# Kernel optimization log

Measured on AMD Instinct MI355X. Metric: run time of the kernel, lower is better.

Reference implementation:

```python
import jax, jax.numpy as jnp
import numpy as np

N, E, G = 50000, 600000, 500          # nodes, edges, graphs in batch
IN_NODE, HID, EDGE = 92, 64, 41       # CGCNN default feature dims
NCONV, PRED, NOUT = 3, 128, 1
Z_DIM = 2 * HID + EDGE                # 169: cat(src_x, dst_x, edge_attr)
BN_EPS = 1e-5


def setup_inputs() -> dict:
    key = jax.random.key(0)
    ks = jax.random.split(key, 14)
    f32 = jnp.float32
    return {
        "x": jax.random.normal(ks[0], (N, IN_NODE), f32),
        "edge_attr": jax.random.normal(ks[1], (E, EDGE), f32),
        "src": jax.random.randint(ks[2], (E,), 0, N),
        "dst": jax.random.randint(ks[3], (E,), 0, N),
        "graph_idx": jnp.sort(jax.random.randint(ks[4], (N,), 0, G)),
        "n_graphs": G,
        "W_embed": jax.random.normal(ks[5], (IN_NODE, HID), f32) / np.sqrt(IN_NODE),
        "b_embed": jnp.zeros((HID,), f32),
        "W_sig": jax.random.normal(ks[6], (NCONV, Z_DIM, HID), f32) / np.sqrt(Z_DIM),
        "b_sig": jnp.zeros((NCONV, HID), f32),
        "W_sp": jax.random.normal(ks[7], (NCONV, Z_DIM, HID), f32) / np.sqrt(Z_DIM),
        "b_sp": jnp.zeros((NCONV, HID), f32),
        "bn_gamma": jnp.ones((NCONV, HID), f32),
        "bn_beta": jnp.zeros((NCONV, HID), f32),
        "W_fc": jax.random.normal(ks[8], (HID, PRED), f32) / np.sqrt(HID),
        "b_fc": jnp.zeros((PRED,), f32),
        "W_out": jax.random.normal(ks[9], (PRED, NOUT), f32) / np.sqrt(PRED),
        "b_out": jnp.zeros((NOUT,), f32),
    }


def reference(x, edge_attr, src, dst, graph_idx, n_graphs,
              W_embed, b_embed, W_sig, b_sig, W_sp, b_sp,
              bn_gamma, bn_beta, W_fc, b_fc, W_out, b_out):
    # node embedding to hidden dim
    h = x @ W_embed + b_embed                                   # [N, HID]
    n_nodes = h.shape[0]
    for i in range(W_sig.shape[0]):
        # per-edge features: gather src/dst node feats + edge feats
        z = jnp.concatenate([h[src], h[dst], edge_attr], axis=1)  # [E, Z_DIM]
        gated = jax.nn.sigmoid(z @ W_sig[i] + b_sig[i])           # [E, HID]
        msg = jax.nn.softplus(z @ W_sp[i] + b_sp[i])              # [E, HID]
        # scatter-sum gated messages into destination node mailboxes
        agg = jax.ops.segment_sum(gated * msg, dst, num_segments=n_nodes)
        h = h + agg                                               # residual
        # batch norm over nodes (training-mode batch stats, biased var)
        mean = h.mean(axis=0)
        var = h.var(axis=0)
        h = (h - mean) * jax.lax.rsqrt(var + BN_EPS) * bn_gamma[i] + bn_beta[i]
    # sum-pool nodes per graph, then dense readout
    graph_feat = jax.ops.segment_sum(h, graph_idx, num_segments=n_graphs)  # [G, HID]
    graph_feat = graph_feat @ W_fc + b_fc                                  # [G, PRED]
    return graph_feat @ W_out + b_out                                      # [G, NOUT]
```

## Files before the change

### kernel.cpp

```cpp
#include <hip/hip_runtime.h>

#define N_NODES 50000
#define N_EDGES 600000
#define N_GRAPHS 500
#define IN_F 92
#define HID 64
#define EDGE_F 41
#define ZDIM 169
#define PRED 128
#define BN_EPS 1e-5f
#define SCAN_BLOCKS 196
#define ROW_U32 24
#define LOG2E 1.4426950408889634f
#define LN2   0.6931471805599453f
#define NAGG_BLOCKS 2048
#define NW2 (NAGG_BLOCKS * 8)
#define PART_T ((N_EDGES + 1 + NW2 - 1) / NW2)

typedef unsigned int u32;
typedef _Float16 f16;
typedef _Float16 f16x2 __attribute__((ext_vector_type(2)));
typedef _Float16 f16x8 __attribute__((ext_vector_type(8)));
typedef float f32x4 __attribute__((ext_vector_type(4)));

__device__ __forceinline__ u32 f2bf(float f) {
    u32 u = __float_as_uint(f);
    return (u + 0x7fffu + ((u >> 16) & 1u)) >> 16;
}

__device__ __forceinline__ int lbound(const int* __restrict__ a, int nelem, int val) {
    int lo = 0, hi = nelem;
    while (lo < hi) {
        int m = (lo + hi) >> 1;
        if (a[m] < val) lo = m + 1; else hi = m;
    }
    return lo;
}

__global__ void k_prep(const float* __restrict__ Wsig, const float* __restrict__ Wsp,
                       const float* __restrict__ Wemb, const int* __restrict__ gidx,
                       f16* __restrict__ Wf16, f16* __restrict__ Wp2,
                       f16* __restrict__ Wef, int* __restrict__ gstart,
                       int* __restrict__ zeroBase) {
    int t = blockIdx.x * 256 + threadIdx.x;
    if (t < 3072) {
        int lane = t & 63;
        int jt = (t >> 6) & 7;
        int kt = (t >> 9) & 1;
        int L = t >> 10;
        int j128 = jt * 16 + (lane & 15);
        const float* Wbase = (j128 < 64) ? Wsig : Wsp;
        int j = j128 & 63;
        f16x8 v;
        #pragma unroll
        for (int b = 0; b < 8; ++b) {
            int k = kt * 32 + (lane >> 4) * 8 + b;
            float f = (k < EDGE_F) ? Wbase[(size_t)L * ZDIM * HID + (128 + k) * HID + j] * LOG2E : 0.f;
            v[b] = (f16)f;
        }
        *(f16x8*)(Wf16 + ((size_t)((L * 2 + kt) * 8 + jt) * 64 + lane) * 8) = v;
    } else if (t < 9216) {
        int t2 = t - 3072;
        int lane = t2 & 63;
        int jt = (t2 >> 6) & 15;
        int kt = (t2 >> 10) & 1;
        int L = t2 >> 11;
        int j256 = jt * 16 + (lane & 15);
        const float* Wbase = (j256 & 64) ? Wsp : Wsig;
        int rowoff = (j256 & 128) ? 64 : 0;
        int j = j256 & 63;
        f16x8 v;
        #pragma unroll
        for (int b = 0; b < 8; ++b) {
            int k = kt * 32 + (lane >> 4) * 8 + b;
            v[b] = (f16)Wbase[(size_t)L * ZDIM * HID + (rowoff + k) * HID + j];
        }
        *(f16x8*)(Wp2 + ((size_t)((L * 2 + kt) * 16 + jt) * 64 + lane) * 8) = v;
    } else if (t < 9984) {
        int t3 = t - 9216;
        int lane = t3 & 63;
        int jt = (t3 >> 6) & 3;
        int kt = t3 >> 8;
        int j = jt * 16 + (lane & 15);
        f16x8 v;
        #pragma unroll
        for (int b = 0; b < 8; ++b) {
            int k = kt * 32 + (lane >> 4) * 8 + b;
            v[b] = (k < IN_F) ? (f16)Wemb[(size_t)k * HID + j] : (f16)0.f;
        }
        *(f16x8*)(Wef + ((size_t)(kt * 4 + jt) * 64 + lane) * 8) = v;
    } else if (t < 10485) {
        int g = t - 9984;
        gstart[g] = lbound(gidx, N_NODES, g);
    } else if (t < 10485 + 2 * N_NODES) {
        zeroBase[t - 10485] = 0;
    }
}

__global__ void k_hist(const int* __restrict__ dst, int* __restrict__ deg) {
    int e = blockIdx.x * 256 + threadIdx.x;
    if (e < N_EDGES) atomicAdd(&deg[dst[e]], 1);
}

__global__ __launch_bounds__(256) void k_scanA(const int* __restrict__ deg,
                                               int* __restrict__ partial) {
    __shared__ int s[256];
    int i = blockIdx.x * 256 + threadIdx.x;
    s[threadIdx.x] = (i < N_NODES) ? deg[i] : 0;
    __syncthreads();
    for (int off = 128; off > 0; off >>= 1) {
        if (threadIdx.x < off) s[threadIdx.x] += s[threadIdx.x + off];
        __syncthreads();
    }
    if (threadIdx.x == 0) partial[blockIdx.x] = s[0];
}

__global__ __launch_bounds__(256) void k_scanB(const int* __restrict__ partial,
                                               int* __restrict__ partialExc,
                                               int* __restrict__ rowptr) {
    __shared__ int s[256];
    int t = threadIdx.x;
    int v = (t < SCAN_BLOCKS) ? partial[t] : 0;
    s[t] = v;
    __syncthreads();
    for (int off = 1; off < 256; off <<= 1) {
        int x = (t >= off) ? s[t - off] : 0;
        __syncthreads();
        s[t] += x;
        __syncthreads();
    }
    partialExc[t] = s[t] - v;
    if (t == 0) rowptr[N_NODES] = N_EDGES;
}

__global__ __launch_bounds__(256) void k_scanC(const int* __restrict__ deg,
                                               const int* __restrict__ partialExc,
                                               int* __restrict__ rowptr) {
    __shared__ int s[256];
    int i = blockIdx.x * 256 + threadIdx.x;
    int t = threadIdx.x;
    int v = (i < N_NODES) ? deg[i] : 0;
    s[t] = v;
    __syncthreads();
    for (int off = 1; off < 256; off <<= 1) {
        int x = (t >= off) ? s[t - off] : 0;
        __syncthreads();
        s[t] += x;
        __syncthreads();
    }
    if (i < N_NODES) rowptr[i] = s[t] - v + partialExc[blockIdx.x];
}

__global__ void k_rank(const int* __restrict__ dst, const int* __restrict__ src,
                       const int* __restrict__ rowptr, int* __restrict__ cursor,
                       int* __restrict__ srcS, int* __restrict__ iperm,
                       int* __restrict__ partW) {
    int e = blockIdx.x * 256 + threadIdx.x;
    if (e <= NW2) partW[e] = min(lbound(rowptr, N_NODES + 1, e * PART_T), N_NODES);
    if (e >= N_EDGES) {
        if (e < N_EDGES + 32) srcS[e] = 0;
        return;
    }
    int d = dst[e];
    int p = rowptr[d] + atomicAdd(&cursor[d], 1);
    srcS[p] = src[e];
    iperm[p] = e;
}

__global__ __launch_bounds__(256) void k_epackS(const float* __restrict__ ea,
                                                const int* __restrict__ iperm,
                                                u32* __restrict__ eapS) {
    const int total = N_EDGES * ROW_U32;
    const int stride = gridDim.x * 256;
    for (int idx = blockIdx.x * 256 + threadIdx.x; idx < total; idx += stride) {
        int p = idx / ROW_U32;
        int q = idx - p * ROW_U32;
        int e = iperm[p];
        int k0 = 2 * q, k1 = k0 + 1;
        float f0 = (k0 < EDGE_F) ? ea[(size_t)e * EDGE_F + k0] : 0.f;
        float f1 = (k1 < EDGE_F) ? ea[(size_t)e * EDGE_F + k1] : 0.f;
        f16x2 hv = {(f16)f0, (f16)f1};
        eapS[idx] = __builtin_bit_cast(u32, hv);
    }
}

__global__ __launch_bounds__(256) void k_embedm(const float* __restrict__ x,
                                                const f16* __restrict__ Wef,
                                                const float* __restrict__ b,
                                                float* __restrict__ A) {
    __shared__ f16x8 Wl[12 * 64];
    for (int i = threadIdx.x; i < 12 * 64; i += 256) Wl[i] = ((const f16x8*)Wef)[i];
    __syncthreads();
    const int lane = threadIdx.x & 63;
    const int col = lane & 15, grp = lane >> 4;
    float bj[4];
    #pragma unroll
    for (int jt = 0; jt < 4; ++jt) bj[jt] = b[jt * 16 + col];
    const int wid = blockIdx.x * 4 + (threadIdx.x >> 6);
    const int nw = gridDim.x * 4;
    for (int c = wid; c < N_NODES / 16; c += nw) {
        const int node = c * 16 + col;
        const float* xr = x + (size_t)node * IN_F;
        f16x8 af[3];
        #pragma unroll
        for (int kt = 0; kt < 3; ++kt) {
            int base = kt * 32 + grp * 8;
            float4 v0 = *(const float4*)(xr + base);
            float4 v1 = (base + 4 < IN_F) ? *(const float4*)(xr + base + 4)
                                          : make_float4(0.f, 0.f, 0.f, 0.f);
            af[kt] = f16x8{(f16)v0.x, (f16)v0.y, (f16)v0.z, (f16)v0.w,
                           (f16)v1.x, (f16)v1.y, (f16)v1.z, (f16)v1.w};
        }
        #pragma unroll
        for (int jt = 0; jt < 4; ++jt) {
            f32x4 c4 = {};
            c4 = __builtin_amdgcn_mfma_f32_16x16x32_f16(af[0], Wl[(0 * 4 + jt) * 64 + lane], c4, 0, 0, 0);
            c4 = __builtin_amdgcn_mfma_f32_16x16x32_f16(af[1], Wl[(1 * 4 + jt) * 64 + lane], c4, 0, 0, 0);
            c4 = __builtin_amdgcn_mfma_f32_16x16x32_f16(af[2], Wl[(2 * 4 + jt) * 64 + lane], c4, 0, 0, 0);
            #pragma unroll
            for (int r = 0; r < 4; ++r)
                A[(size_t)(c * 16 + grp * 4 + r) * HID + jt * 16 + col] = c4[r] + bj[jt];
        }
    }
}

__global__ __launch_bounds__(256, 4) void k_projm(const float* __restrict__ A,
                                                  const float* __restrict__ statsPrev,
                                                  const float* __restrict__ gammaP,
                                                  const float* __restrict__ betaP,
                                                  int applyBN,
                                                  const f16* __restrict__ Wp2L,
                                                  const float* __restrict__ bsig,
                                                  const float* __restrict__ bsp,
                                                  u32* __restrict__ pA,
                                                  u32* __restrict__ pB,
                                                  float* __restrict__ statsOut) {
    __shared__ f16x8 Wl[32 * 64];
    for (int i = threadIdx.x; i < 32 * 64; i += 256) Wl[i] = ((const f16x8*)Wp2L)[i];
    if (blockIdx.x == 0)
        for (int i = threadIdx.x; i < 128 * 32; i += 256) statsOut[i] = 0.f;
    __syncthreads();
    const int lane = threadIdx.x & 63;
    const int col = lane & 15;
    float sck[2][8], shk[2][8];
    #pragma unroll
    for (int kt = 0; kt < 2; ++kt)
        #pragma unroll
        for (int b = 0; b < 8; ++b) {
            int k = kt * 32 + (lane >> 4) * 8 + b;
            float scv = 1.f, shv = 0.f;
            if (applyBN) {
                float m = statsPrev[k * 32] * (1.f / N_NODES);
                float v = statsPrev[(64 + k) * 32] * (1.f / N_NODES) - m * m;
                scv = rsqrtf(v + BN_EPS) * gammaP[k];
                shv = betaP[k] - m * scv;
            }
            sck[kt][b] = scv;
            shk[kt][b] = shv;
        }
    float bAs[4], bPs[4];
    #pragma unroll
    for (int jt = 0; jt < 4; ++jt) {
        bAs[jt] = bsig[jt * 16 + col] * LOG2E;
        bPs[jt] = bsp[jt * 16 + col] * LOG2E;
    }
    const int wid = blockIdx.x * 4 + (threadIdx.x >> 6);
    const int nw = gridDim.x * 4;
    for (int c = wid; c < N_NODES / 16; c += nw) {
        const int node = c * 16 + col;
        const float4* Arow = (const float4*)(A + (size_t)node * HID);
        f16x8 af[2];
        #pragma unroll
        for (int kt = 0; kt < 2; ++kt) {
            float4 v0 = Arow[kt * 8 + (lane >> 4) * 2];
            float4 v1 = Arow[kt * 8 + (lane >> 4) * 2 + 1];
            float e0 = v0.x * sck[kt][0] + shk[kt][0];
            float e1 = v0.y * sck[kt][1] + shk[kt][1];
            float e2 = v0.z * sck[kt][2] + shk[kt][2];
            float e3 = v0.w * sck[kt][3] + shk[kt][3];
            float e4 = v1.x * sck[kt][4] + shk[kt][4];
            float e5 = v1.y * sck[kt][5] + shk[kt][5];
            float e6 = v1.z * sck[kt][6] + shk[kt][6];
            float e7 = v1.w * sck[kt][7] + shk[kt][7];
            af[kt] = f16x8{(f16)e0, (f16)e1, (f16)e2, (f16)e3,
                           (f16)e4, (f16)e5, (f16)e6, (f16)e7};
        }
        #pragma unroll
        for (int h = 0; h < 2; ++h) {
            f32x4 c4[8];
            #pragma unroll
            for (int jt2 = 0; jt2 < 8; ++jt2) {
                int jt = h * 8 + jt2;
                f32x4 acc = {};
                acc = __builtin_amdgcn_mfma_f32_16x16x32_f16(af[0], Wl[(0 * 16 + jt) * 64 + lane], acc, 0, 0, 0);
                c4[jt2] = __builtin_amdgcn_mfma_f32_16x16x32_f16(af[1], Wl[(1 * 16 + jt) * 64 + lane], acc, 0, 0, 0);
            }
            u32* dstArr = h ? pB : pA;
            #pragma unroll
            for (int jt2 = 0; jt2 < 4; ++jt2)
                #pragma unroll
                for (int r = 0; r < 4; ++r) {
                    float s = fmaf(c4[jt2][r], LOG2E, h ? 0.f : bAs[jt2]);
                    float p = fmaf(c4[jt2 + 4][r], LOG2E, h ? 0.f : bPs[jt2]);
                    int n2 = c * 16 + (lane >> 4) * 4 + r;
                    dstArr[(size_t)n2 * HID + jt2 * 16 + col] = f2bf(s) | (f2bf(p) << 16);
                }
        }
    }
}


#define CTX_DECL_INIT(S, widx)                                                \
    int n##S = __builtin_amdgcn_readfirstlane(partW[widx]);                   \
    const int ne##S = __builtin_amdgcn_readfirstlane(partW[(widx) + 1]);      \
    bool act##S = n##S < ne##S;                                               \
    int rb##S = 0, re##S = 0;                                                 \
    float resid##S = 0.f;                                                     \
    float bsg##S[4], bsp##S[4], accv##S[4];                                   \
    int s0##S = 0, s1##S = 0, s2##S = 0, s3##S = 0;                           \
    {                                                                         \
        _Pragma("unroll")                                                     \
        for (int jt = 0; jt < 4; ++jt) {                                      \
            bsg##S[jt] = 0.f; bsp##S[jt] = 0.f; accv##S[jt] = 0.f;            \
        }                                                                     \
        if (act##S) {                                                         \
            rb##S = __builtin_amdgcn_readfirstlane(rowptr[n##S]);             \
            re##S = __builtin_amdgcn_readfirstlane(rowptr[n##S + 1]);         \
            resid##S = A[(size_t)n##S * HID + lane];                          \
            if (applyBN) resid##S = resid##S * scL + shL;                     \
            _Pragma("unroll")                                                 \
            for (int jt = 0; jt < 4; ++jt) {                                  \
                u32 pb = pBv[(size_t)n##S * HID + jt * 16 + col];             \
                bsg##S[jt] = __uint_as_float(pb << 16);                       \
                bsp##S[jt] = __uint_as_float(pb & 0xffff0000u);               \
            }                                                                 \
            const int* sp = srcS + rb##S + rowb;                              \
            s0##S = sp[0]; s1##S = sp[1]; s2##S = sp[2]; s3##S = sp[3];       \
        }                                                                     \
    }

#define STEP_LOADS(S)                                                         \
    u32 ga##S[4][4];                                                          \
    f16x8 a0##S, a1##S;                                                       \
    if (act##S) {                                                             \
        const u32* g0##S = pAv + (size_t)s0##S * HID + col;                   \
        const u32* g1##S = pAv + (size_t)s1##S * HID + col;                   \
        const u32* g2##S = pAv + (size_t)s2##S * HID + col;                   \
        const u32* g3##S = pAv + (size_t)s3##S * HID + col;                   \
        _Pragma("unroll")                                                     \
        for (int jt = 0; jt < 4; ++jt) {                                      \
            ga##S[jt][0] = g0##S[jt * 16];                                    \
            ga##S[jt][1] = g1##S[jt * 16];                                    \
            ga##S[jt][2] = g2##S[jt * 16];                                    \
            ga##S[jt][3] = g3##S[jt * 16];                                    \
        }                                                                     \
        const f16x8* arow##S = (const f16x8*)(eapS + (size_t)(rb##S + col) * ROW_U32); \
        a0##S = arow##S[grp];                                                 \
        a1##S = arow##S[4 + grp];                                             \
    }

#define STEP_COMPUTE(S)                                                       \
    if (act##S) {                                                             \
        const int cnt##S = re##S - rb##S;                                     \
        if (cnt##S > 0) {                                                     \
            _Pragma("unroll")                                                 \
            for (int jt = 0; jt < 4; ++jt) {                                  \
                f32x4 cs = {bsg##S[jt], bsg##S[jt], bsg##S[jt], bsg##S[jt]};  \
                f32x4 cp = {bsp##S[jt], bsp##S[jt], bsp##S[jt], bsp##S[jt]};  \
                f16x8 w0s = Wlds[(jt) * 64 + lane];                           \
                f16x8 w1s = Wlds[(8 + jt) * 64 + lane];                       \
                f16x8 w0p = Wlds[(4 + jt) * 64 + lane];                       \
                f16x8 w1p = Wlds[(12 + jt) * 64 + lane];                      \
                cs = __builtin_amdgcn_mfma_f32_16x16x32_f16(a0##S, w0s, cs, 0, 0, 0); \
                cs = __builtin_amdgcn_mfma_f32_16x16x32_f16(a1##S, w1s, cs, 0, 0, 0); \
                cp = __builtin_amdgcn_mfma_f32_16x16x32_f16(a0##S, w0p, cp, 0, 0, 0); \
                cp = __builtin_amdgcn_mfma_f32_16x16x32_f16(a1##S, w1p, cp, 0, 0, 0); \
                _Pragma("unroll")                                             \
                for (int r = 0; r < 4; ++r) {                                 \
                    float s_ = cs[r] + __uint_as_float(ga##S[jt][r] << 16);   \
                    float p_ = cp[r] + __uint_as_float(ga##S[jt][r] & 0xffff0000u); \
                    float g_ = __builtin_amdgcn_rcpf(1.f + exp2f(-s_));       \
                    float m_ = fmaxf(p_, 0.f) + log2f(1.f + exp2f(-fabsf(p_))); \
                    accv##S[jt] += (rowb + r < cnt##S) ? g_ * m_ : 0.f;       \
                }                                                             \
            }                                                                 \
            rb##S += 16;                                                      \
        }                                                                     \
        while (rb##S >= re##S) {                                              \
            _Pragma("unroll")                                                 \
            for (int jt = 0; jt < 4; ++jt) {                                  \
                accv##S[jt] += __shfl_xor(accv##S[jt], 16);                   \
                accv##S[jt] += __shfl_xor(accv##S[jt], 32);                   \
            }                                                                 \
            float accSel = (lane & 32) ? ((lane & 16) ? accv##S[3] : accv##S[2]) \
                                       : ((lane & 16) ? accv##S[1] : accv##S[0]); \
            float outv = resid##S + accSel * LN2;                             \
            Aout[(size_t)n##S * HID + lane] = outv;                           \
            lsum += outv;                                                     \
            lsq += outv * outv;                                               \
            accv##S[0] = accv##S[1] = accv##S[2] = accv##S[3] = 0.f;          \
            rb##S = re##S;                                                    \
            ++n##S;                                                           \
            if (n##S >= ne##S) { act##S = false; break; }                     \
            re##S = __builtin_amdgcn_readfirstlane(rowptr[n##S + 1]);         \
            resid##S = A[(size_t)n##S * HID + lane];                          \
            if (applyBN) resid##S = resid##S * scL + shL;                     \
            _Pragma("unroll")                                                 \
            for (int jt = 0; jt < 4; ++jt) {                                  \
                u32 pb = pBv[(size_t)n##S * HID + jt * 16 + col];             \
                bsg##S[jt] = __uint_as_float(pb << 16);                       \
                bsp##S[jt] = __uint_as_float(pb & 0xffff0000u);               \
            }                                                                 \
        }                                                                     \
        if (act##S) {                                                         \
            const int* sp##S = srcS + rb##S + rowb;                           \
            s0##S = sp##S[0]; s1##S = sp##S[1];                               \
            s2##S = sp##S[2]; s3##S = sp##S[3];                               \
        }                                                                     \
    }

__global__ __launch_bounds__(256, 4) void k_nodeagg(const float* __restrict__ A,
                                                    const float* __restrict__ statsPrev,
                                                    const float* __restrict__ gammaP,
                                                    const float* __restrict__ betaP,
                                                    int applyBN,
                                                    const u32* __restrict__ pAv,
                                                    const u32* __restrict__ pBv,
                                                    const u32* __restrict__ eapS,
                                                    const int* __restrict__ srcS,
                                                    const int* __restrict__ rowptr,
                                                    const int* __restrict__ partW,
                                                    const f16* __restrict__ Wf16L,
                                                    float* __restrict__ Aout,
                                                    float* __restrict__ statsOut) {
    __shared__ f16x8 Wlds[16 * 64];
    __shared__ float redS[256], redQ[256];
    for (int i = threadIdx.x; i < 16 * 64; i += 256)
        Wlds[i] = ((const f16x8*)Wf16L)[i];

    const int lane = threadIdx.x & 63;
    const int col = lane & 15;
    const int grp = lane >> 4;
    const int rowb = grp * 4;

    float scL = 1.f, shL = 0.f;
    if (applyBN) {
        float m = statsPrev[lane * 32] * (1.f / N_NODES);
        float v = statsPrev[(64 + lane) * 32] * (1.f / N_NODES) - m * m;
        scL = rsqrtf(v + BN_EPS) * gammaP[lane];
        shL = betaP[lane] - m * scL;
    }
    __syncthreads();

    const int w2 = (((blockIdx.x << 2) + (threadIdx.x >> 6)) << 1);
    float lsum = 0.f, lsq = 0.f;

    CTX_DECL_INIT(A, w2)
    CTX_DECL_INIT(B, w2 + 1)

    while (actA || actB) {
        STEP_LOADS(A)
        STEP_LOADS(B)
        STEP_COMPUTE(A)
        STEP_COMPUTE(B)
    }

    redS[threadIdx.x] = lsum;
    redQ[threadIdx.x] = lsq;
    __syncthreads();
    if (threadIdx.x < 64) {
        float s = redS[threadIdx.x] + redS[threadIdx.x + 64] + redS[threadIdx.x + 128] + redS[threadIdx.x + 192];
        float q = redQ[threadIdx.x] + redQ[threadIdx.x + 64] + redQ[threadIdx.x + 128] + redQ[threadIdx.x + 192];
        unsafeAtomicAdd(&statsOut[threadIdx.x * 32], s);
        unsafeAtomicAdd(&statsOut[(64 + threadIdx.x) * 32], q);
    }
}

__global__ __launch_bounds__(256) void k_poolout(const float* __restrict__ A,
                                                 const float* __restrict__ stats,
                                                 const float* __restrict__ gamma,
                                                 const float* __restrict__ beta,
                                                 const int* __restrict__ gstart,
                                                 const float* __restrict__ Wfc,
                                                 const float* __restrict__ bfc,
                                                 const float* __restrict__ Wout,
                                                 const float* __restrict__ bout,
                                                 float* __restrict__ out) {
    const int g = blockIdx.x;
    const int lane = threadIdx.x & 63;
    const int wv = threadIdx.x >> 6;
    const int rb = gstart[g], re = gstart[g + 1];
    float s = 0.f;
    for (int r = rb + wv; r < re; r += 4) s += A[(size_t)r * HID + lane];
    __shared__ float red[4][64];
    __shared__ float gfeat[64];
    red[wv][lane] = s;
    __syncthreads();
    if (threadIdx.x < 64) {
        float t = red[0][lane] + red[1][lane] + red[2][lane] + red[3][lane];
        float m = stats[lane * 32] * (1.f / N_NODES);
        float v = stats[(64 + lane) * 32] * (1.f / N_NODES) - m * m;
        float scv = rsqrtf(v + BN_EPS) * gamma[lane];
        float shv = beta[lane] - m * scv;
        gfeat[lane] = scv * t + shv * (float)(re - rb);
    }
    __syncthreads();
    __shared__ float r2[128];
    if (threadIdx.x < 128) {
        float p = bfc[threadIdx.x];
        #pragma unroll 8
        for (int k = 0; k < 64; ++k) p += gfeat[k] * Wfc[k * PRED + threadIdx.x];
        r2[threadIdx.x] = p * Wout[threadIdx.x];
    }
    __syncthreads();
    if (threadIdx.x < 64) {
        float v2 = r2[threadIdx.x] + r2[threadIdx.x + 64];
        #pragma unroll
        for (int off = 32; off > 0; off >>= 1) v2 += __shfl_down(v2, off);
        if (threadIdx.x == 0) out[g] = v2 + bout[0];
    }
}

extern "C" void kernel_launch(void* const* d_in, const int* in_sizes, int n_in,
                              void* d_out, int out_size, void* d_ws, size_t ws_size,
                              hipStream_t stream) {
    const float* x         = (const float*)d_in[0];
    const float* edge_attr = (const float*)d_in[1];
    const int*   src       = (const int*)d_in[2];
    const int*   dst       = (const int*)d_in[3];
    const int*   gidx      = (const int*)d_in[4];
    const float* W_embed   = (const float*)d_in[6];
    const float* b_embed   = (const float*)d_in[7];
    const float* W_sig     = (const float*)d_in[8];
    const float* b_sig     = (const float*)d_in[9];
    const float* W_sp      = (const float*)d_in[10];
    const float* b_sp      = (const float*)d_in[11];
    const float* bn_gamma  = (const float*)d_in[12];
    const float* bn_beta   = (const float*)d_in[13];
    const float* W_fc      = (const float*)d_in[14];
    const float* b_fc      = (const float*)d_in[15];
    const float* W_out     = (const float*)d_in[16];
    const float* b_out     = (const float*)d_in[17];
    float* out = (float*)d_out;

    const size_t NH = (size_t)N_NODES * HID;
    float* ws     = (float*)d_ws;
    float* A      = ws;
    u32*   pA     = (u32*)(A + NH);
    u32*   pB     = pA + NH;
    u32*   eapS   = pB + NH;
    int*   srcS   = (int*)(eapS + (size_t)(N_EDGES + 32) * ROW_U32);
    int*   iperm  = srcS + N_EDGES + 32;
    int*   rowptr = iperm + N_EDGES;
    int*   deg    = rowptr + N_NODES + 1;
    int*   cursor = deg + N_NODES;
    int*   partial    = cursor + N_NODES;
    int*   partialExc = partial + 256;
    int*   partW  = partialExc + 256;
    int*   gstart = partW + NW2 + 2;
    f16*   Wf16   = (f16*)(((size_t)(gstart + 504) + 15) & ~(size_t)15);
    f16*   Wp2    = Wf16 + 3 * 2 * 8 * 64 * 8;
    f16*   Wef    = Wp2 + 3 * 2 * 16 * 64 * 8;
    float* stats  = (float*)(Wef + 3 * 4 * 64 * 8);

    k_prep<<<(10485 + 2 * N_NODES + 255) / 256, 256, 0, stream>>>(
        W_sig, W_sp, W_embed, gidx, Wf16, Wp2, Wef, gstart, deg);
    k_hist<<<(N_EDGES + 255) / 256, 256, 0, stream>>>(dst, deg);
    k_scanA<<<SCAN_BLOCKS, 256, 0, stream>>>(deg, partial);
    k_scanB<<<1, 256, 0, stream>>>(partial, partialExc, rowptr);
    k_scanC<<<SCAN_BLOCKS, 256, 0, stream>>>(deg, partialExc, rowptr);
    k_rank<<<(N_EDGES + 32 + 255) / 256, 256, 0, stream>>>(dst, src, rowptr, cursor,
                                                           srcS, iperm, partW);
    k_embedm<<<512, 256, 0, stream>>>(x, Wef, b_embed, A);
    k_epackS<<<4096, 256, 0, stream>>>(edge_attr, iperm, eapS);

    for (int i = 0; i < 3; ++i) {
        const float* stPrev = stats + (size_t)(i > 0 ? i - 1 : 0) * 4096;
        const float* gP     = bn_gamma + (i > 0 ? i - 1 : 0) * HID;
        const float* bP     = bn_beta + (i > 0 ? i - 1 : 0) * HID;
        float* stOut        = stats + (size_t)i * 4096;
        int applyBN = (i > 0) ? 1 : 0;
        k_projm<<<512, 256, 0, stream>>>(A, stPrev, gP, bP, applyBN,
                                         Wp2 + (size_t)i * 2 * 16 * 64 * 8,
                                         b_sig + i * HID, b_sp + i * HID,
                                         pA, pB, stOut);
        k_nodeagg<<<NAGG_BLOCKS, 256, 0, stream>>>(A, stPrev, gP, bP, applyBN,
                                                   pA, pB, eapS, srcS, rowptr, partW,
                                                   Wf16 + (size_t)i * 2 * 8 * 64 * 8,
                                                   A, stOut);
    }

    k_poolout<<<N_GRAPHS, 256, 0, stream>>>(A, stats + 2 * 4096, bn_gamma + 2 * HID,
                                            bn_beta + 2 * HID, gstart,
                                            W_fc, b_fc, W_out, b_out, out);
}
```

Measured before the change: 502.8 us.

## Fuse scan stages and pack edge attributes directly in the rank kernel

Removes the single-block middle scan kernel: each scanC block now sums the preceding block partials itself with a wave reduction. The separate edge-attribute packing kernel and the iperm array are dropped; k_rank converts each edge's row to fp16 and writes it with 16-byte stores straight to its sorted position. This saves two launches and the iperm round trip. In exchange, each thread reads its edge row with strided per-thread loads that coalesce poorly, and scanC blocks redundantly re-sum up to 196 partials.

```diff
diff --git a/kernel.cpp b/kernel.cpp
--- a/kernel.cpp
+++ b/kernel.cpp
@@ -41,7 +41,7 @@
                        const float* __restrict__ Wemb, const int* __restrict__ gidx,
                        f16* __restrict__ Wf16, f16* __restrict__ Wp2,
                        f16* __restrict__ Wef, int* __restrict__ gstart,
-                       int* __restrict__ zeroBase) {
+                       int* __restrict__ rowptr, int* __restrict__ zeroBase) {
     int t = blockIdx.x * 256 + threadIdx.x;
     if (t < 3072) {
         int lane = t & 63;
@@ -92,6 +92,7 @@
     } else if (t < 10485) {
         int g = t - 9984;
         gstart[g] = lbound(gidx, N_NODES, g);
+        if (g == 0) rowptr[N_NODES] = N_EDGES;
     } else if (t < 10485 + 2 * N_NODES) {
         zeroBase[t - 10485] = 0;
     }
@@ -115,12 +116,21 @@
     if (threadIdx.x == 0) partial[blockIdx.x] = s[0];
 }
 
-__global__ __launch_bounds__(256) void k_scanB(const int* __restrict__ partial,
-                                               int* __restrict__ partialExc,
+__global__ __launch_bounds__(256) void k_scanC(const int* __restrict__ deg,
+                                               const int* __restrict__ partial,
                                                int* __restrict__ rowptr) {
     __shared__ int s[256];
+    __shared__ int base;
+    int i = blockIdx.x * 256 + threadIdx.x;
     int t = threadIdx.x;
-    int v = (t < SCAN_BLOCKS) ? partial[t] : 0;
+    if (t < 64) {
+        int acc = 0;
+        for (int j = t; j < blockIdx.x; j += 64) acc += partial[j];
+        #pragma unroll
+        for (int off = 32; off > 0; off >>= 1) acc += __shfl_xor(acc, off);
+        if (t == 0) base = acc;
+    }
+    int v = (i < N_NODES) ? deg[i] : 0;
     s[t] = v;
     __syncthreads();
     for (int off = 1; off < 256; off <<= 1) {
@@ -129,31 +139,13 @@
         s[t] += x;
         __syncthreads();
     }
-    partialExc[t] = s[t] - v;
-    if (t == 0) rowptr[N_NODES] = N_EDGES;
-}
-
-__global__ __launch_bounds__(256) void k_scanC(const int* __restrict__ deg,
-                                               const int* __restrict__ partialExc,
-                                               int* __restrict__ rowptr) {
-    __shared__ int s[256];
-    int i = blockIdx.x * 256 + threadIdx.x;
-    int t = threadIdx.x;
-    int v = (i < N_NODES) ? deg[i] : 0;
-    s[t] = v;
-    __syncthreads();
-    for (int off = 1; off < 256; off <<= 1) {
-        int x = (t >= off) ? s[t - off] : 0;
-        __syncthreads();
-        s[t] += x;
-        __syncthreads();
-    }
-    if (i < N_NODES) rowptr[i] = s[t] - v + partialExc[blockIdx.x];
+    if (i < N_NODES) rowptr[i] = s[t] - v + base;
 }
 
 __global__ void k_rank(const int* __restrict__ dst, const int* __restrict__ src,
+                       const float* __restrict__ ea,
                        const int* __restrict__ rowptr, int* __restrict__ cursor,
-                       int* __restrict__ srcS, int* __restrict__ iperm,
+                       int* __restrict__ srcS, u32* __restrict__ eapS,
                        int* __restrict__ partW) {
     int e = blockIdx.x * 256 + threadIdx.x;
     if (e <= NW2) partW[e] = min(lbound(rowptr, N_NODES + 1, e * PART_T), N_NODES);
@@ -164,24 +156,19 @@
     int d = dst[e];
     int p = rowptr[d] + atomicAdd(&cursor[d], 1);
     srcS[p] = src[e];
-    iperm[p] = e;
-}
-
-__global__ __launch_bounds__(256) void k_epackS(const float* __restrict__ ea,
-                                                const int* __restrict__ iperm,
-                                                u32* __restrict__ eapS) {
-    const int total = N_EDGES * ROW_U32;
-    const int stride = gridDim.x * 256;
-    for (int idx = blockIdx.x * 256 + threadIdx.x; idx < total; idx += stride) {
-        int p = idx / ROW_U32;
-        int q = idx - p * ROW_U32;
-        int e = iperm[p];
+    const float* row = ea + (size_t)e * EDGE_F;
+    u32 buf[ROW_U32];
+    #pragma unroll
+    for (int q = 0; q < ROW_U32; ++q) {
         int k0 = 2 * q, k1 = k0 + 1;
-        float f0 = (k0 < EDGE_F) ? ea[(size_t)e * EDGE_F + k0] : 0.f;
-        float f1 = (k1 < EDGE_F) ? ea[(size_t)e * EDGE_F + k1] : 0.f;
-        f16x2 hv = {(f16)f0, (f16)f1};
-        eapS[idx] = __builtin_bit_cast(u32, hv);
-    }
+        f16x2 hv = {(f16)((k0 < EDGE_F) ? row[k0] : 0.f),
+                    (f16)((k1 < EDGE_F) ? row[k1] : 0.f)};
+        buf[q] = __builtin_bit_cast(u32, hv);
+    }
+    uint4* orow = (uint4*)(eapS + (size_t)p * ROW_U32);
+    #pragma unroll
+    for (int q4 = 0; q4 < ROW_U32 / 4; ++q4)
+        orow[q4] = make_uint4(buf[4 * q4], buf[4 * q4 + 1], buf[4 * q4 + 2], buf[4 * q4 + 3]);
 }
 
 __global__ __launch_bounds__(256) void k_embedm(const float* __restrict__ x,
@@ -550,13 +537,11 @@
     u32*   pB     = pA + NH;
     u32*   eapS   = pB + NH;
     int*   srcS   = (int*)(eapS + (size_t)(N_EDGES + 32) * ROW_U32);
-    int*   iperm  = srcS + N_EDGES + 32;
-    int*   rowptr = iperm + N_EDGES;
+    int*   rowptr = srcS + N_EDGES + 32;
     int*   deg    = rowptr + N_NODES + 1;
     int*   cursor = deg + N_NODES;
     int*   partial    = cursor + N_NODES;
-    int*   partialExc = partial + 256;
-    int*   partW  = partialExc + 256;
+    int*   partW  = partial + 256;
     int*   gstart = partW + NW2 + 2;
     f16*   Wf16   = (f16*)(((size_t)(gstart + 504) + 15) & ~(size_t)15);
     f16*   Wp2    = Wf16 + 3 * 2 * 8 * 64 * 8;
@@ -564,15 +549,13 @@
     float* stats  = (float*)(Wef + 3 * 4 * 64 * 8);
 
     k_prep<<<(10485 + 2 * N_NODES + 255) / 256, 256, 0, stream>>>(
-        W_sig, W_sp, W_embed, gidx, Wf16, Wp2, Wef, gstart, deg);
+        W_sig, W_sp, W_embed, gidx, Wf16, Wp2, Wef, gstart, rowptr, deg);
     k_hist<<<(N_EDGES + 255) / 256, 256, 0, stream>>>(dst, deg);
     k_scanA<<<SCAN_BLOCKS, 256, 0, stream>>>(deg, partial);
-    k_scanB<<<1, 256, 0, stream>>>(partial, partialExc, rowptr);
-    k_scanC<<<SCAN_BLOCKS, 256, 0, stream>>>(deg, partialExc, rowptr);
-    k_rank<<<(N_EDGES + 32 + 255) / 256, 256, 0, stream>>>(dst, src, rowptr, cursor,
-                                                           srcS, iperm, partW);
+    k_scanC<<<SCAN_BLOCKS, 256, 0, stream>>>(deg, partial, rowptr);
+    k_rank<<<(N_EDGES + 32 + 255) / 256, 256, 0, stream>>>(dst, src, edge_attr, rowptr,
+                                                           cursor, srcS, eapS, partW);
     k_embedm<<<512, 256, 0, stream>>>(x, Wef, b_embed, A);
-    k_epackS<<<4096, 256, 0, stream>>>(edge_attr, iperm, eapS);
 
     for (int i = 0; i < 3; ++i) {
         const float* stPrev = stats + (size_t)(i > 0 ? i - 1 : 0) * 4096;
```

Result: faster. 478.1 us, median of 2 (-4.9%).
